# Performance work log

Hardware: AMD Instinct MI355X
Metric: run time of the kernel (lower is better)

## Reference

```python
import jax, jax.numpy as jnp
import numpy as np

C = 64
CQ = C // 8


def setup_inputs() -> dict:
    key = jax.random.key(0)
    ks = jax.random.split(key, 8)
    x = jax.random.normal(ks[0], (8, C, 64, 64), dtype=jnp.float32)
    s = 1.0 / np.sqrt(C)
    Wq = jax.random.normal(ks[1], (CQ, C), dtype=jnp.float32) * s
    bq = jax.random.normal(ks[2], (CQ,), dtype=jnp.float32) * s
    Wk = jax.random.normal(ks[3], (CQ, C), dtype=jnp.float32) * s
    bk = jax.random.normal(ks[4], (CQ,), dtype=jnp.float32) * s
    Wv = jax.random.normal(ks[5], (C, C), dtype=jnp.float32) * s
    bv = jax.random.normal(ks[6], (C,), dtype=jnp.float32) * s
    gamma = jnp.array([0.5], dtype=jnp.float32)  # nonzero so value path contributes
    return {"x": x, "Wq": Wq, "bq": bq, "Wk": Wk, "bk": bk, "Wv": Wv, "bv": bv, "gamma": gamma}


def reference(x, Wq, bq, Wk, bk, Wv, bv, gamma):
    B, Cc, H, W = x.shape
    xf = x.reshape(B, Cc, H * W)  # [B, C, N]
    # 1x1 conv == channel-mixing linear
    f = jnp.einsum('oc,bcn->bon', Wq, xf) + bq[None, :, None]  # [B, C/8, N]
    g = jnp.einsum('oc,bcn->bon', Wk, xf) + bk[None, :, None]  # [B, C/8, N]
    h = jnp.einsum('oc,bcn->bon', Wv, xf) + bv[None, :, None]  # [B, C, N]
    # scores[b,i,j] = f[b,:,i] . g[b,:,j]; softmax over dim=1 (query dim i)
    scores = jnp.einsum('bdi,bdj->bij', f, g)  # [B, N, N]
    beta = jax.nn.softmax(scores, axis=1)
    o = gamma[0] * jnp.einsum('bcn,bnm->bcm', h, beta) + xf
    return o.reshape(B, Cc, H, W)
```

## Files before the change

### kernel.cpp

```cpp
#include <hip/hip_runtime.h>
#include <hip/hip_fp16.h>


typedef _Float16 half8_t __attribute__((ext_vector_type(8)));
typedef _Float16 half4_t __attribute__((ext_vector_type(4)));
typedef _Float16 half2_t __attribute__((ext_vector_type(2)));
typedef __fp16  fp16x2  __attribute__((ext_vector_type(2)));
typedef float float4_t __attribute__((ext_vector_type(4)));

#define NTOK 4096
#define PRH 72
#define LOG2E 1.44269504088896340736f

#if __has_builtin(__builtin_amdgcn_exp2f)
__device__ __forceinline__ float fexp2(float x) { return __builtin_amdgcn_exp2f(x); }
#else
__device__ __forceinline__ float fexp2(float x) { return exp2f(x); }
#endif

__device__ __forceinline__ half2_t pkcvt(float a, float b) {
    fp16x2 v = __builtin_amdgcn_cvt_pkrtz(a, b);
    return __builtin_bit_cast(half2_t, v);
}

__global__ __launch_bounds__(320) void proj_kernel(
    const float* __restrict__ x,
    const float* __restrict__ Wq, const float* __restrict__ bq,
    const float* __restrict__ Wk, const float* __restrict__ bk,
    const float* __restrict__ Wv, const float* __restrict__ bv,
    __half* __restrict__ fTR, __half* __restrict__ gT16, __half* __restrict__ hM)
{
    __shared__ float xl[64 * 64];
    const int t  = threadIdx.x;
    const int kt = blockIdx.x;
    const int b  = blockIdx.y;
    const int n0 = kt * 64;

    if (t < 256) {
        const int f4 = t & 15;
        const int cb = t >> 4;
#pragma unroll
        for (int i = 0; i < 4; i++) {
            const int c = cb + i * 16;
            float4 v = *(const float4*)(x + (((size_t)(b * 64 + c)) << 12) + n0 + f4 * 4);
            *(float4*)(&xl[c * 64 + f4 * 4]) = v;
        }
    }
    __syncthreads();

    const int w    = t >> 6;
    const int lane = t & 63;
    const int n    = n0 + lane;
    float acc[16];

    if (w == 0) {
#pragma unroll
        for (int j = 0; j < 8; j++) { acc[j] = bq[j]; acc[8 + j] = bk[j]; }
        for (int c = 0; c < 64; c++) {
            const float xc = xl[c * 64 + lane];
#pragma unroll
            for (int j = 0; j < 8; j++) {
                acc[j]     += Wq[j * 64 + c] * xc;
                acc[8 + j] += Wk[j * 64 + c] * xc;
            }
        }
        float gn2 = 0.f;
#pragma unroll
        for (int j = 0; j < 8; j++) gn2 += acc[8 + j] * acc[8 + j];
        const float M = (LOG2E * 4.6f) * __builtin_sqrtf(gn2) + 1.0f;

        const int t4 = lane >> 4, ml = lane & 15;
        half4_t flo = {(_Float16)(acc[0] * LOG2E), (_Float16)(acc[1] * LOG2E),
                       (_Float16)(acc[2] * LOG2E), (_Float16)(acc[3] * LOG2E)};
        half4_t fhi = {(_Float16)(acc[4] * LOG2E), (_Float16)(acc[5] * LOG2E),
                       (_Float16)(acc[6] * LOG2E), (_Float16)(acc[7] * LOG2E)};
        __half* fb = fTR + ((size_t)b << 15) + (size_t)(kt * 16 + ml) * 32 + t4 * 4;
        *(half4_t*)fb        = flo;
        *(half4_t*)(fb + 16) = fhi;

        half8_t glo, gpad;
#pragma unroll
        for (int j = 0; j < 8; j++) glo[j] = (_Float16)acc[8 + j];
        gpad = (half8_t){};
        gpad[0] = (_Float16)(-M);
        __half* gp = gT16 + (size_t)((b << 12) + n) * 16;
        *(half8_t*)gp       = glo;
        *(half8_t*)(gp + 8) = gpad;
    } else {
        const int ch0 = (w - 1) * 16;
#pragma unroll
        for (int j = 0; j < 16; j++) acc[j] = bv[ch0 + j];
        for (int c = 0; c < 64; c++) {
            const float xc = xl[c * 64 + lane];
#pragma unroll
            for (int j = 0; j < 16; j++) acc[j] += Wv[(ch0 + j) * 64 + c] * xc;
        }
#pragma unroll
        for (int j = 0; j < 16; j++)
            hM[(((size_t)b * 64 + ch0 + j) << 12) + n] = __float2half(acc[j]);
    }
}

template<int NT>
__global__ __launch_bounds__(256) void attn_kernel(
    const __half* __restrict__ fTR, const __half* __restrict__ gT16,
    const __half* __restrict__ hM,
    __half* __restrict__ Pacc, float* __restrict__ Lsum)
{
    __shared__ __align__(16) _Float16 hl[2][64 * PRH];
    const int tid   = threadIdx.x;
    const int w     = tid >> 6;
    const int lane  = tid & 63;
    const int q     = lane >> 4;
    const int ml    = lane & 15;
    const int b     = blockIdx.y;
    const int split = blockIdx.z;
    const int col   = blockIdx.x * 64 + w * 16 + ml;
    const bool qlo  = (q < 2);

    half4_t gfrag = *(const half4_t*)(gT16 + ((size_t)((b << 12) + col)) * 16 + q * 4);

    float4_t acc[4];
#pragma unroll
    for (int cg = 0; cg < 4; cg++) acc[cg] = (float4_t){0.f, 0.f, 0.f, 0.f};
    float ls0 = 0.f, ls1 = 0.f, ls2 = 0.f, ls3 = 0.f;

    const int kt0 = split * NT;
    const int c0  = tid >> 3;
    const int g0  = tid & 7;

    const __half* srow0 = hM + ((size_t)(b * 64 + c0) << 12) + kt0 * 64 + g0 * 8;
    const __half* srow1 = srow0 + ((size_t)32 << 12);
    const __half* fptr  = fTR + ((size_t)b << 15) + (size_t)(kt0 * 16 + ml) * 32 + q * 16;

    half4_t padv = (half4_t){};
    if (q == 2) padv[0] = (_Float16)1.0f;

    uint4 s0 = *(const uint4*)srow0;
    uint4 s1 = *(const uint4*)srow1;
    half4_t afn0 = padv, afn1 = padv, afn2 = padv, afn3 = padv;
    if (qlo) {
        afn0 = *(const half4_t*)(fptr);
        afn1 = *(const half4_t*)(fptr + 4);
        afn2 = *(const half4_t*)(fptr + 8);
        afn3 = *(const half4_t*)(fptr + 12);
    }
    *(uint4*)(&hl[0][c0 * PRH + g0 * 8])        = s0;
    *(uint4*)(&hl[0][(c0 + 32) * PRH + g0 * 8]) = s1;
    __syncthreads();

#pragma unroll 1
    for (int kt = 0; kt < NT; kt++) {
        const _Float16* hbL = &hl[kt & 1][ml * PRH + q * 4];

        float4_t st0 = __builtin_amdgcn_mfma_f32_16x16x16f16(
            afn0, gfrag, (float4_t){0.f, 0.f, 0.f, 0.f}, 0, 0, 0);
        float4_t st1 = __builtin_amdgcn_mfma_f32_16x16x16f16(
            afn1, gfrag, (float4_t){0.f, 0.f, 0.f, 0.f}, 0, 0, 0);
        float4_t st2 = __builtin_amdgcn_mfma_f32_16x16x16f16(
            afn2, gfrag, (float4_t){0.f, 0.f, 0.f, 0.f}, 0, 0, 0);
        float4_t st3 = __builtin_amdgcn_mfma_f32_16x16x16f16(
            afn3, gfrag, (float4_t){0.f, 0.f, 0.f, 0.f}, 0, 0, 0);

        if (kt + 1 < NT) {
            if (qlo) {
                afn0 = *(const half4_t*)(fptr + 512);
                afn1 = *(const half4_t*)(fptr + 516);
                afn2 = *(const half4_t*)(fptr + 520);
                afn3 = *(const half4_t*)(fptr + 524);
            }
            s0 = *(const uint4*)(srow0 + 64);
            s1 = *(const uint4*)(srow1 + 64);
            fptr  += 512;
            srow0 += 64;
            srow1 += 64;
        }

        {
            float p0 = fexp2(st0[0]), p1 = fexp2(st0[1]),
                  p2 = fexp2(st0[2]), p3 = fexp2(st0[3]);
            ls0 += p0; ls1 += p1; ls2 += p2; ls3 += p3;
            half2_t plo = pkcvt(p0, p1), phi = pkcvt(p2, p3);
            half4_t pf = {plo[0], plo[1], phi[0], phi[1]};
#pragma unroll
            for (int cg = 0; cg < 4; cg++)
                acc[cg] = __builtin_amdgcn_mfma_f32_16x16x16f16(
                    *(const half4_t*)(hbL + cg * (16 * PRH) + 0 * 16), pf, acc[cg], 0, 0, 0);
        }
        {
            float p0 = fexp2(st1[0]), p1 = fexp2(st1[1]),
                  p2 = fexp2(st1[2]), p3 = fexp2(st1[3]);
            ls0 += p0; ls1 += p1; ls2 += p2; ls3 += p3;
            half2_t plo = pkcvt(p0, p1), phi = pkcvt(p2, p3);
            half4_t pf = {plo[0], plo[1], phi[0], phi[1]};
#pragma unroll
            for (int cg = 0; cg < 4; cg++)
                acc[cg] = __builtin_amdgcn_mfma_f32_16x16x16f16(
                    *(const half4_t*)(hbL + cg * (16 * PRH) + 1 * 16), pf, acc[cg], 0, 0, 0);
        }
        {
            float p0 = fexp2(st2[0]), p1 = fexp2(st2[1]),
                  p2 = fexp2(st2[2]), p3 = fexp2(st2[3]);
            ls0 += p0; ls1 += p1; ls2 += p2; ls3 += p3;
            half2_t plo = pkcvt(p0, p1), phi = pkcvt(p2, p3);
            half4_t pf = {plo[0], plo[1], phi[0], phi[1]};
#pragma unroll
            for (int cg = 0; cg < 4; cg++)
                acc[cg] = __builtin_amdgcn_mfma_f32_16x16x16f16(
                    *(const half4_t*)(hbL + cg * (16 * PRH) + 2 * 16), pf, acc[cg], 0, 0, 0);
        }
        {
            float p0 = fexp2(st3[0]), p1 = fexp2(st3[1]),
                  p2 = fexp2(st3[2]), p3 = fexp2(st3[3]);
            ls0 += p0; ls1 += p1; ls2 += p2; ls3 += p3;
            half2_t plo = pkcvt(p0, p1), phi = pkcvt(p2, p3);
            half4_t pf = {plo[0], plo[1], phi[0], phi[1]};
#pragma unroll
            for (int cg = 0; cg < 4; cg++)
                acc[cg] = __builtin_amdgcn_mfma_f32_16x16x16f16(
                    *(const half4_t*)(hbL + cg * (16 * PRH) + 3 * 16), pf, acc[cg], 0, 0, 0);
        }

        if (kt + 1 < NT) {
            _Float16* hn = &hl[(kt + 1) & 1][0];
            *(uint4*)(&hn[c0 * PRH + g0 * 8])        = s0;
            *(uint4*)(&hn[(c0 + 32) * PRH + g0 * 8]) = s1;
        }
        __syncthreads();
    }

    float l = (ls0 + ls1) + (ls2 + ls3);
    l += __shfl_xor(l, 16, 64);
    l += __shfl_xor(l, 32, 64);

    __half* pa = Pacc + (((size_t)(split * 8 + b) * 64) << 12);
#pragma unroll
    for (int cg = 0; cg < 4; cg++)
#pragma unroll
        for (int r = 0; r < 4; r++) {
            int ch = cg * 16 + q * 4 + r;
            pa[((size_t)ch << 12) + col] = __float2half(acc[cg][r]);
        }
    if (q == 0)
        Lsum[((size_t)(split * 8 + b) << 12) + col] = l;
}

template<int S>
__global__ __launch_bounds__(256) void merge_kernel(
    const __half* __restrict__ Pacc, const float* __restrict__ Lsum,
    const float* __restrict__ x, const float* __restrict__ gammap,
    float* __restrict__ out)
{
    __shared__ float invL[64];
    const int tid  = threadIdx.x;
    const int c4   = tid & 15;
    const int chh  = tid >> 4;
    const int b    = blockIdx.y;
    const int col0 = blockIdx.x * 64;
    const int ch   = blockIdx.z * 16 + chh;

    if (tid < 64) {
        float L = 0.f;
#pragma unroll
        for (int s = 0; s < S; s++)
            L += Lsum[((size_t)(s * 8 + b) << 12) + col0 + tid];
        invL[tid] = gammap[0] / L;
    }
    __syncthreads();

    const int cc = c4 * 4;
    const size_t base = (((size_t)b * 64 + ch) << 12) + col0 + cc;
    float4 xv = *(const float4*)(x + base);
    float o0 = 0.f, o1 = 0.f, o2 = 0.f, o3 = 0.f;
#pragma unroll
    for (int s = 0; s < S; s++) {
        half4_t pv = *(const half4_t*)(Pacc +
            (((size_t)(s * 8 + b) * 64 + ch) << 12) + col0 + cc);
        o0 += (float)pv[0];
        o1 += (float)pv[1];
        o2 += (float)pv[2];
        o3 += (float)pv[3];
    }
    float4 ov;
    ov.x = o0 * invL[cc]     + xv.x;
    ov.y = o1 * invL[cc + 1] + xv.y;
    ov.z = o2 * invL[cc + 2] + xv.z;
    ov.w = o3 * invL[cc + 3] + xv.w;
    *(float4*)(out + base) = ov;
}

extern "C" void kernel_launch(void* const* d_in, const int* in_sizes, int n_in,
                              void* d_out, int out_size, void* d_ws, size_t ws_size,
                              hipStream_t stream) {
    const float* x     = (const float*)d_in[0];
    const float* Wq    = (const float*)d_in[1];
    const float* bq    = (const float*)d_in[2];
    const float* Wk    = (const float*)d_in[3];
    const float* bk    = (const float*)d_in[4];
    const float* Wv    = (const float*)d_in[5];
    const float* bv    = (const float*)d_in[6];
    const float* gamma = (const float*)d_in[7];
    float* out = (float*)d_out;

    const size_t fr_bytes  = (size_t)8 * 32768 * 2;
    const size_t g_bytes   = (size_t)8 * NTOK * 16 * 2;
    const size_t hM_bytes  = (size_t)8 * 64 * NTOK * 2;
    const size_t pa_split  = (size_t)8 * 64 * NTOK * 2;
    const size_t l_split   = (size_t)8 * NTOK * sizeof(float);
    const size_t base_need = fr_bytes + g_bytes + hM_bytes;

    int S = 1;
    if (ws_size >= base_need + 4 * (pa_split + l_split)) S = 4;
    else if (ws_size >= base_need + 2 * (pa_split + l_split)) S = 2;

    char* p = (char*)d_ws;
    __half* fTR  = (__half*)p;  p += fr_bytes;
    __half* gT16 = (__half*)p;  p += g_bytes;
    __half* hM   = (__half*)p;  p += hM_bytes;
    __half* Pacc = (__half*)p;  p += (size_t)S * pa_split;
    float*  Lsum = (float*)p;

    proj_kernel<<<dim3(64, 8), 320, 0, stream>>>(x, Wq, bq, Wk, bk, Wv, bv,
                                                 fTR, gT16, hM);
    if (S == 4) {
        attn_kernel<16><<<dim3(64, 8, 4), 256, 0, stream>>>(fTR, gT16, hM, Pacc, Lsum);
        merge_kernel<4><<<dim3(64, 8, 4), 256, 0, stream>>>(Pacc, Lsum, x, gamma, out);
    } else if (S == 2) {
        attn_kernel<32><<<dim3(64, 8, 2), 256, 0, stream>>>(fTR, gT16, hM, Pacc, Lsum);
        merge_kernel<2><<<dim3(64, 8, 4), 256, 0, stream>>>(Pacc, Lsum, x, gamma, out);
    } else {
        attn_kernel<64><<<dim3(64, 8, 1), 256, 0, stream>>>(fTR, gT16, hM, Pacc, Lsum);
        merge_kernel<1><<<dim3(64, 8, 4), 256, 0, stream>>>(Pacc, Lsum, x, gamma, out);
    }
}
```

Measured before the change: 137.8 us.

## Process two column tiles per attention block to reuse f and h loads

Each attention block now computes two 64-column output tiles (A and B), sharing the f fragments and the LDS h tiles across both. This halves the grid and the redundant global and LDS traffic per output column. The cost is doubled accumulator and score registers, which may lower occupancy. The merge kernel also moves to 8-wide half loads with half as many z-blocks, and the projection kernel prefetches the next x value from LDS.

```diff
diff --git a/kernel.cpp b/kernel.cpp
--- a/kernel.cpp
+++ b/kernel.cpp
@@ -56,13 +56,15 @@
     if (w == 0) {
 #pragma unroll
         for (int j = 0; j < 8; j++) { acc[j] = bq[j]; acc[8 + j] = bk[j]; }
+        float xc = xl[lane];
         for (int c = 0; c < 64; c++) {
-            const float xc = xl[c * 64 + lane];
+            const float xn = (c < 63) ? xl[(c + 1) * 64 + lane] : 0.f;
 #pragma unroll
             for (int j = 0; j < 8; j++) {
                 acc[j]     += Wq[j * 64 + c] * xc;
                 acc[8 + j] += Wk[j * 64 + c] * xc;
             }
+            xc = xn;
         }
         float gn2 = 0.f;
 #pragma unroll
@@ -90,10 +92,12 @@
         const int ch0 = (w - 1) * 16;
 #pragma unroll
         for (int j = 0; j < 16; j++) acc[j] = bv[ch0 + j];
+        float xc = xl[lane];
         for (int c = 0; c < 64; c++) {
-            const float xc = xl[c * 64 + lane];
+            const float xn = (c < 63) ? xl[(c + 1) * 64 + lane] : 0.f;
 #pragma unroll
             for (int j = 0; j < 16; j++) acc[j] += Wv[(ch0 + j) * 64 + c] * xc;
+            xc = xn;
         }
 #pragma unroll
         for (int j = 0; j < 16; j++)
@@ -115,15 +119,21 @@
     const int ml    = lane & 15;
     const int b     = blockIdx.y;
     const int split = blockIdx.z;
-    const int col   = blockIdx.x * 64 + w * 16 + ml;
+    const int colA  = blockIdx.x * 128 + w * 16 + ml;
+    const int colB  = colA + 64;
     const bool qlo  = (q < 2);
 
-    half4_t gfrag = *(const half4_t*)(gT16 + ((size_t)((b << 12) + col)) * 16 + q * 4);
-
-    float4_t acc[4];
-#pragma unroll
-    for (int cg = 0; cg < 4; cg++) acc[cg] = (float4_t){0.f, 0.f, 0.f, 0.f};
-    float ls0 = 0.f, ls1 = 0.f, ls2 = 0.f, ls3 = 0.f;
+    half4_t gfA = *(const half4_t*)(gT16 + ((size_t)((b << 12) + colA)) * 16 + q * 4);
+    half4_t gfB = *(const half4_t*)(gT16 + ((size_t)((b << 12) + colB)) * 16 + q * 4);
+
+    float4_t accA[4], accB[4];
+#pragma unroll
+    for (int cg = 0; cg < 4; cg++) {
+        accA[cg] = (float4_t){0.f, 0.f, 0.f, 0.f};
+        accB[cg] = (float4_t){0.f, 0.f, 0.f, 0.f};
+    }
+    float lsA0 = 0.f, lsA1 = 0.f, lsA2 = 0.f, lsA3 = 0.f;
+    float lsB0 = 0.f, lsB1 = 0.f, lsB2 = 0.f, lsB3 = 0.f;
 
     const int kt0 = split * NT;
     const int c0  = tid >> 3;
@@ -153,14 +163,22 @@
     for (int kt = 0; kt < NT; kt++) {
         const _Float16* hbL = &hl[kt & 1][ml * PRH + q * 4];
 
-        float4_t st0 = __builtin_amdgcn_mfma_f32_16x16x16f16(
-            afn0, gfrag, (float4_t){0.f, 0.f, 0.f, 0.f}, 0, 0, 0);
-        float4_t st1 = __builtin_amdgcn_mfma_f32_16x16x16f16(
-            afn1, gfrag, (float4_t){0.f, 0.f, 0.f, 0.f}, 0, 0, 0);
-        float4_t st2 = __builtin_amdgcn_mfma_f32_16x16x16f16(
-            afn2, gfrag, (float4_t){0.f, 0.f, 0.f, 0.f}, 0, 0, 0);
-        float4_t st3 = __builtin_amdgcn_mfma_f32_16x16x16f16(
-            afn3, gfrag, (float4_t){0.f, 0.f, 0.f, 0.f}, 0, 0, 0);
+        float4_t stA0 = __builtin_amdgcn_mfma_f32_16x16x16f16(
+            afn0, gfA, (float4_t){0.f, 0.f, 0.f, 0.f}, 0, 0, 0);
+        float4_t stA1 = __builtin_amdgcn_mfma_f32_16x16x16f16(
+            afn1, gfA, (float4_t){0.f, 0.f, 0.f, 0.f}, 0, 0, 0);
+        float4_t stA2 = __builtin_amdgcn_mfma_f32_16x16x16f16(
+            afn2, gfA, (float4_t){0.f, 0.f, 0.f, 0.f}, 0, 0, 0);
+        float4_t stA3 = __builtin_amdgcn_mfma_f32_16x16x16f16(
+            afn3, gfA, (float4_t){0.f, 0.f, 0.f, 0.f}, 0, 0, 0);
+        float4_t stB0 = __builtin_amdgcn_mfma_f32_16x16x16f16(
+            afn0, gfB, (float4_t){0.f, 0.f, 0.f, 0.f}, 0, 0, 0);
+        float4_t stB1 = __builtin_amdgcn_mfma_f32_16x16x16f16(
+            afn1, gfB, (float4_t){0.f, 0.f, 0.f, 0.f}, 0, 0, 0);
+        float4_t stB2 = __builtin_amdgcn_mfma_f32_16x16x16f16(
+            afn2, gfB, (float4_t){0.f, 0.f, 0.f, 0.f}, 0, 0, 0);
+        float4_t stB3 = __builtin_amdgcn_mfma_f32_16x16x16f16(
+            afn3, gfB, (float4_t){0.f, 0.f, 0.f, 0.f}, 0, 0, 0);
 
         if (kt + 1 < NT) {
             if (qlo) {
@@ -177,48 +195,76 @@
         }
 
         {
-            float p0 = fexp2(st0[0]), p1 = fexp2(st0[1]),
-                  p2 = fexp2(st0[2]), p3 = fexp2(st0[3]);
-            ls0 += p0; ls1 += p1; ls2 += p2; ls3 += p3;
-            half2_t plo = pkcvt(p0, p1), phi = pkcvt(p2, p3);
-            half4_t pf = {plo[0], plo[1], phi[0], phi[1]};
-#pragma unroll
-            for (int cg = 0; cg < 4; cg++)
-                acc[cg] = __builtin_amdgcn_mfma_f32_16x16x16f16(
-                    *(const half4_t*)(hbL + cg * (16 * PRH) + 0 * 16), pf, acc[cg], 0, 0, 0);
+            float pA0 = fexp2(stA0[0]), pA1 = fexp2(stA0[1]),
+                  pA2 = fexp2(stA0[2]), pA3 = fexp2(stA0[3]);
+            float pB0 = fexp2(stB0[0]), pB1 = fexp2(stB0[1]),
+                  pB2 = fexp2(stB0[2]), pB3 = fexp2(stB0[3]);
+            lsA0 += pA0; lsA1 += pA1; lsA2 += pA2; lsA3 += pA3;
+            lsB0 += pB0; lsB1 += pB1; lsB2 += pB2; lsB3 += pB3;
+            half2_t a_lo = pkcvt(pA0, pA1), a_hi = pkcvt(pA2, pA3);
+            half2_t b_lo = pkcvt(pB0, pB1), b_hi = pkcvt(pB2, pB3);
+            half4_t pfA = {a_lo[0], a_lo[1], a_hi[0], a_hi[1]};
+            half4_t pfB = {b_lo[0], b_lo[1], b_hi[0], b_hi[1]};
+#pragma unroll
+            for (int cg = 0; cg < 4; cg++) {
+                half4_t ah = *(const half4_t*)(hbL + cg * (16 * PRH) + 0 * 16);
+                accA[cg] = __builtin_amdgcn_mfma_f32_16x16x16f16(ah, pfA, accA[cg], 0, 0, 0);
+                accB[cg] = __builtin_amdgcn_mfma_f32_16x16x16f16(ah, pfB, accB[cg], 0, 0, 0);
+            }
         }
         {
-            float p0 = fexp2(st1[0]), p1 = fexp2(st1[1]),
-                  p2 = fexp2(st1[2]), p3 = fexp2(st1[3]);
-            ls0 += p0; ls1 += p1; ls2 += p2; ls3 += p3;
-            half2_t plo = pkcvt(p0, p1), phi = pkcvt(p2, p3);
-            half4_t pf = {plo[0], plo[1], phi[0], phi[1]};
-#pragma unroll
-            for (int cg = 0; cg < 4; cg++)
-                acc[cg] = __builtin_amdgcn_mfma_f32_16x16x16f16(
-                    *(const half4_t*)(hbL + cg * (16 * PRH) + 1 * 16), pf, acc[cg], 0, 0, 0);
+            float pA0 = fexp2(stA1[0]), pA1 = fexp2(stA1[1]),
+                  pA2 = fexp2(stA1[2]), pA3 = fexp2(stA1[3]);
+            float pB0 = fexp2(stB1[0]), pB1 = fexp2(stB1[1]),
+                  pB2 = fexp2(stB1[2]), pB3 = fexp2(stB1[3]);
+            lsA0 += pA0; lsA1 += pA1; lsA2 += pA2; lsA3 += pA3;
+            lsB0 += pB0; lsB1 += pB1; lsB2 += pB2; lsB3 += pB3;
+            half2_t a_lo = pkcvt(pA0, pA1), a_hi = pkcvt(pA2, pA3);
+            half2_t b_lo = pkcvt(pB0, pB1), b_hi = pkcvt(pB2, pB3);
+            half4_t pfA = {a_lo[0], a_lo[1], a_hi[0], a_hi[1]};
+            half4_t pfB = {b_lo[0], b_lo[1], b_hi[0], b_hi[1]};
+#pragma unroll
+            for (int cg = 0; cg < 4; cg++) {
+                half4_t ah = *(const half4_t*)(hbL + cg * (16 * PRH) + 1 * 16);
+                accA[cg] = __builtin_amdgcn_mfma_f32_16x16x16f16(ah, pfA, accA[cg], 0, 0, 0);
+                accB[cg] = __builtin_amdgcn_mfma_f32_16x16x16f16(ah, pfB, accB[cg], 0, 0, 0);
+            }
         }
         {
-            float p0 = fexp2(st2[0]), p1 = fexp2(st2[1]),
-                  p2 = fexp2(st2[2]), p3 = fexp2(st2[3]);
-            ls0 += p0; ls1 += p1; ls2 += p2; ls3 += p3;
-            half2_t plo = pkcvt(p0, p1), phi = pkcvt(p2, p3);
-            half4_t pf = {plo[0], plo[1], phi[0], phi[1]};
-#pragma unroll
-            for (int cg = 0; cg < 4; cg++)
-                acc[cg] = __builtin_amdgcn_mfma_f32_16x16x16f16(
-                    *(const half4_t*)(hbL + cg * (16 * PRH) + 2 * 16), pf, acc[cg], 0, 0, 0);
+            float pA0 = fexp2(stA2[0]), pA1 = fexp2(stA2[1]),
+                  pA2 = fexp2(stA2[2]), pA3 = fexp2(stA2[3]);
+            float pB0 = fexp2(stB2[0]), pB1 = fexp2(stB2[1]),
+                  pB2 = fexp2(stB2[2]), pB3 = fexp2(stB2[3]);
+            lsA0 += pA0; lsA1 += pA1; lsA2 += pA2; lsA3 += pA3;
+            lsB0 += pB0; lsB1 += pB1; lsB2 += pB2; lsB3 += pB3;
+            half2_t a_lo = pkcvt(pA0, pA1), a_hi = pkcvt(pA2, pA3);
+            half2_t b_lo = pkcvt(pB0, pB1), b_hi = pkcvt(pB2, pB3);
+            half4_t pfA = {a_lo[0], a_lo[1], a_hi[0], a_hi[1]};
+            half4_t pfB = {b_lo[0], b_lo[1], b_hi[0], b_hi[1]};
+#pragma unroll
+            for (int cg = 0; cg < 4; cg++) {
+                half4_t ah = *(const half4_t*)(hbL + cg * (16 * PRH) + 2 * 16);
+                accA[cg] = __builtin_amdgcn_mfma_f32_16x16x16f16(ah, pfA, accA[cg], 0, 0, 0);
+                accB[cg] = __builtin_amdgcn_mfma_f32_16x16x16f16(ah, pfB, accB[cg], 0, 0, 0);
+            }
         }
         {
-            float p0 = fexp2(st3[0]), p1 = fexp2(st3[1]),
-                  p2 = fexp2(st3[2]), p3 = fexp2(st3[3]);
-            ls0 += p0; ls1 += p1; ls2 += p2; ls3 += p3;
-            half2_t plo = pkcvt(p0, p1), phi = pkcvt(p2, p3);
-            half4_t pf = {plo[0], plo[1], phi[0], phi[1]};
-#pragma unroll
-            for (int cg = 0; cg < 4; cg++)
-                acc[cg] = __builtin_amdgcn_mfma_f32_16x16x16f16(
-                    *(const half4_t*)(hbL + cg * (16 * PRH) + 3 * 16), pf, acc[cg], 0, 0, 0);
+            float pA0 = fexp2(stA3[0]), pA1 = fexp2(stA3[1]),
+                  pA2 = fexp2(stA3[2]), pA3 = fexp2(stA3[3]);
+            float pB0 = fexp2(stB3[0]), pB1 = fexp2(stB3[1]),
+                  pB2 = fexp2(stB3[2]), pB3 = fexp2(stB3[3]);
+            lsA0 += pA0; lsA1 += pA1; lsA2 += pA2; lsA3 += pA3;
+            lsB0 += pB0; lsB1 += pB1; lsB2 += pB2; lsB3 += pB3;
+            half2_t a_lo = pkcvt(pA0, pA1), a_hi = pkcvt(pA2, pA3);
+            half2_t b_lo = pkcvt(pB0, pB1), b_hi = pkcvt(pB2, pB3);
+            half4_t pfA = {a_lo[0], a_lo[1], a_hi[0], a_hi[1]};
+            half4_t pfB = {b_lo[0], b_lo[1], b_hi[0], b_hi[1]};
+#pragma unroll
+            for (int cg = 0; cg < 4; cg++) {
+                half4_t ah = *(const half4_t*)(hbL + cg * (16 * PRH) + 3 * 16);
+                accA[cg] = __builtin_amdgcn_mfma_f32_16x16x16f16(ah, pfA, accA[cg], 0, 0, 0);
+                accB[cg] = __builtin_amdgcn_mfma_f32_16x16x16f16(ah, pfB, accB[cg], 0, 0, 0);
+            }
         }
 
         if (kt + 1 < NT) {
@@ -229,9 +275,12 @@
         __syncthreads();
     }
 
-    float l = (ls0 + ls1) + (ls2 + ls3);
-    l += __shfl_xor(l, 16, 64);
-    l += __shfl_xor(l, 32, 64);
+    float lA = (lsA0 + lsA1) + (lsA2 + lsA3);
+    lA += __shfl_xor(lA, 16, 64);
+    lA += __shfl_xor(lA, 32, 64);
+    float lB = (lsB0 + lsB1) + (lsB2 + lsB3);
+    lB += __shfl_xor(lB, 16, 64);
+    lB += __shfl_xor(lB, 32, 64);
 
     __half* pa = Pacc + (((size_t)(split * 8 + b) * 64) << 12);
 #pragma unroll
@@ -239,10 +288,13 @@
 #pragma unroll
         for (int r = 0; r < 4; r++) {
             int ch = cg * 16 + q * 4 + r;
-            pa[((size_t)ch << 12) + col] = __float2half(acc[cg][r]);
-        }
-    if (q == 0)
-        Lsum[((size_t)(split * 8 + b) << 12) + col] = l;
+            pa[((size_t)ch << 12) + colA] = __float2half(accA[cg][r]);
+            pa[((size_t)ch << 12) + colB] = __float2half(accB[cg][r]);
+        }
+    if (q == 0) {
+        Lsum[((size_t)(split * 8 + b) << 12) + colA] = lA;
+        Lsum[((size_t)(split * 8 + b) << 12) + colB] = lB;
+    }
 }
 
 template<int S>
@@ -253,11 +305,11 @@
 {
     __shared__ float invL[64];
     const int tid  = threadIdx.x;
-    const int c4   = tid & 15;
-    const int chh  = tid >> 4;
+    const int oc   = tid & 7;
+    const int chl  = tid >> 3;
     const int b    = blockIdx.y;
     const int col0 = blockIdx.x * 64;
-    const int ch   = blockIdx.z * 16 + chh;
+    const int ch   = blockIdx.z * 32 + chl;
 
     if (tid < 64) {
         float L = 0.f;
@@ -268,25 +320,31 @@
     }
     __syncthreads();
 
-    const int cc = c4 * 4;
+    const int cc = oc * 8;
     const size_t base = (((size_t)b * 64 + ch) << 12) + col0 + cc;
-    float4 xv = *(const float4*)(x + base);
-    float o0 = 0.f, o1 = 0.f, o2 = 0.f, o3 = 0.f;
+    float o[8];
+#pragma unroll
+    for (int i = 0; i < 8; i++) o[i] = 0.f;
 #pragma unroll
     for (int s = 0; s < S; s++) {
-        half4_t pv = *(const half4_t*)(Pacc +
+        half8_t pv = *(const half8_t*)(Pacc +
             (((size_t)(s * 8 + b) * 64 + ch) << 12) + col0 + cc);
-        o0 += (float)pv[0];
-        o1 += (float)pv[1];
-        o2 += (float)pv[2];
-        o3 += (float)pv[3];
-    }
-    float4 ov;
-    ov.x = o0 * invL[cc]     + xv.x;
-    ov.y = o1 * invL[cc + 1] + xv.y;
-    ov.z = o2 * invL[cc + 2] + xv.z;
-    ov.w = o3 * invL[cc + 3] + xv.w;
-    *(float4*)(out + base) = ov;
+#pragma unroll
+        for (int i = 0; i < 8; i++) o[i] += (float)pv[i];
+    }
+    float4 x0 = *(const float4*)(x + base);
+    float4 x1 = *(const float4*)(x + base + 4);
+    float4 v0, v1;
+    v0.x = o[0] * invL[cc]     + x0.x;
+    v0.y = o[1] * invL[cc + 1] + x0.y;
+    v0.z = o[2] * invL[cc + 2] + x0.z;
+    v0.w = o[3] * invL[cc + 3] + x0.w;
+    v1.x = o[4] * invL[cc + 4] + x1.x;
+    v1.y = o[5] * invL[cc + 5] + x1.y;
+    v1.z = o[6] * invL[cc + 6] + x1.z;
+    v1.w = o[7] * invL[cc + 7] + x1.w;
+    *(float4*)(out + base)     = v0;
+    *(float4*)(out + base + 4) = v1;
 }
 
 extern "C" void kernel_launch(void* const* d_in, const int* in_sizes, int n_in,
@@ -323,13 +381,13 @@
     proj_kernel<<<dim3(64, 8), 320, 0, stream>>>(x, Wq, bq, Wk, bk, Wv, bv,
                                                  fTR, gT16, hM);
     if (S == 4) {
-        attn_kernel<16><<<dim3(64, 8, 4), 256, 0, stream>>>(fTR, gT16, hM, Pacc, Lsum);
-        merge_kernel<4><<<dim3(64, 8, 4), 256, 0, stream>>>(Pacc, Lsum, x, gamma, out);
+        attn_kernel<16><<<dim3(32, 8, 4), 256, 0, stream>>>(fTR, gT16, hM, Pacc, Lsum);
+        merge_kernel<4><<<dim3(64, 8, 2), 256, 0, stream>>>(Pacc, Lsum, x, gamma, out);
     } else if (S == 2) {
-        attn_kernel<32><<<dim3(64, 8, 2), 256, 0, stream>>>(fTR, gT16, hM, Pacc, Lsum);
-        merge_kernel<2><<<dim3(64, 8, 4), 256, 0, stream>>>(Pacc, Lsum, x, gamma, out);
+        attn_kernel<32><<<dim3(32, 8, 2), 256, 0, stream>>>(fTR, gT16, hM, Pacc, Lsum);
+        merge_kernel<2><<<dim3(64, 8, 2), 256, 0, stream>>>(Pacc, Lsum, x, gamma, out);
     } else {
-        attn_kernel<64><<<dim3(64, 8, 1), 256, 0, stream>>>(fTR, gT16, hM, Pacc, Lsum);
-        merge_kernel<1><<<dim3(64, 8, 4), 256, 0, stream>>>(Pacc, Lsum, x, gamma, out);
-    }
-}
+        attn_kernel<64><<<dim3(32, 8, 1), 256, 0, stream>>>(fTR, gT16, hM, Pacc, Lsum);
+        merge_kernel<1><<<dim3(64, 8, 2), 256, 0, stream>>>(Pacc, Lsum, x, gamma, out);
+    }
+}
```

Result: no change. 136.3 us (-1.1%).
